# Kernel optimization log

Measured on AMD Instinct MI355X. Metric: run time of the kernel, lower is better.

The kernel has to match this reference:

```python
import jax, jax.numpy as jnp
import numpy as np

HIDDEN = 4096
NQ = 32        # query heads
NKV = 8        # kv heads
HD = 128       # head dim
EPS = 1e-6
BASE = 10000.0
T = 2048


def setup_inputs() -> dict:
    key = jax.random.key(0)
    ks = jax.random.split(key, 4)
    s = 0.02
    return {
        "hidden_states": jax.random.normal(ks[0], (T, HIDDEN), jnp.float32),
        "w_qkv": jax.random.normal(ks[1], ((NQ + 2 * NKV) * HD, HIDDEN), jnp.float32) * s,
        "q_norm_w": jnp.ones((HD,), jnp.float32),
        "k_norm_w": jnp.ones((HD,), jnp.float32),
        "w_o": jax.random.normal(ks[2], (HIDDEN, NQ * HD), jnp.float32) * s,
        "positions": jnp.arange(T, dtype=jnp.int64),
    }


def _rms_norm(x, w):
    # x: [T, H, D], normalize over last dim
    var = jnp.mean(jnp.square(x), axis=-1, keepdims=True)
    return x * jax.lax.rsqrt(var + EPS) * w


def _rope(x, positions):
    # neox-style: split halves. x: [T, H, D]
    half = HD // 2
    inv_freq = 1.0 / (BASE ** (jnp.arange(0, HD, 2, dtype=jnp.float32) / HD))  # [half]
    ang = positions.astype(jnp.float32)[:, None] * inv_freq  # [T, half]
    cos = jnp.cos(ang)[:, None, :]  # [T, 1, half]
    sin = jnp.sin(ang)[:, None, :]
    x1, x2 = x[..., :half], x[..., half:]
    return jnp.concatenate([x1 * cos - x2 * sin, x2 * cos + x1 * sin], axis=-1)


def reference(hidden_states, w_qkv, q_norm_w, k_norm_w, w_o, positions):
    t = hidden_states.shape[0]
    qkv = hidden_states @ w_qkv.T  # [T, (NQ+2*NKV)*HD]
    q, k, v = jnp.split(qkv, [NQ * HD, (NQ + NKV) * HD], axis=-1)
    q = _rms_norm(q.reshape(t, NQ, HD), q_norm_w)
    k = _rms_norm(k.reshape(t, NKV, HD), k_norm_w)
    v = v.reshape(t, NKV, HD)
    q = _rope(q, positions)
    k = _rope(k, positions)

    g = NQ // NKV
    qg = q.reshape(t, NKV, g, HD).transpose(1, 2, 0, 3)  # [NKV, g, T, HD]
    kt = k.transpose(1, 0, 2)  # [NKV, T, HD]
    vt = v.transpose(1, 0, 2)
    scale = HD ** -0.5
    scores = jnp.einsum('hgqd,hkd->hgqk', qg, kt) * scale  # [NKV, g, T, T]
    causal = positions[:, None] >= positions[None, :]  # [T, T]
    scores = jnp.where(causal[None, None], scores, jnp.float32(-1e30))
    p = jax.nn.softmax(scores, axis=-1)
    o = jnp.einsum('hgqk,hkd->hgqd', p, vt)  # [NKV, g, T, HD]
    o = o.transpose(2, 0, 1, 3).reshape(t, NQ * HD)
    return o @ w_o.T
```

## Files before the change

### kernel.cpp

```cpp
#include <hip/hip_runtime.h>
#include <hip/hip_bf16.h>

typedef float f32x4 __attribute__((ext_vector_type(4)));
typedef short s16x8 __attribute__((ext_vector_type(8)));
typedef short s16x4 __attribute__((ext_vector_type(4)));
typedef unsigned short u16;

#define HIDDEN 4096
#define NQ 32
#define NKV 8
#define HD 128
#define T_SEQ 2048
#define QKV_N ((NQ + 2 * NKV) * HD)

__device__ __forceinline__ u16 f2bf(float f) {
    union { float f; unsigned u; } v; v.f = f;
    unsigned r = v.u + 0x7FFFu + ((v.u >> 16) & 1u);
    return (u16)(r >> 16);
}
__device__ __forceinline__ float b2f(u16 h) {
    union { unsigned u; float f; } v; v.u = ((unsigned)h) << 16; return v.f;
}
__device__ __forceinline__ void gload_lds16(const u16* g, u16* l) {
    __builtin_amdgcn_global_load_lds(
        (const __attribute__((address_space(1))) unsigned int*)g,
        (__attribute__((address_space(3))) unsigned int*)l,
        16, 0, 0);
}
__device__ __forceinline__ int xcd_swz(int flat, int nwg) {
    return (flat & 7) * (nwg >> 3) + (flat >> 3);
}

__device__ __forceinline__ void conv8(const float* src, u16* dst, int i) {
    const float4 a = ((const float4*)src)[2 * i];
    const float4 b = ((const float4*)src)[2 * i + 1];
    s16x8 o;
    o[0] = (short)f2bf(a.x); o[1] = (short)f2bf(a.y);
    o[2] = (short)f2bf(a.z); o[3] = (short)f2bf(a.w);
    o[4] = (short)f2bf(b.x); o[5] = (short)f2bf(b.y);
    o[6] = (short)f2bf(b.z); o[7] = (short)f2bf(b.w);
    ((s16x8*)dst)[i] = o;
}
__global__ __launch_bounds__(256) void conv2_bf16_kern(
    const float* __restrict__ s1, u16* __restrict__ d1, int n1,
    const float* __restrict__ s2, u16* __restrict__ d2, int n2)
{
    for (int i = blockIdx.x * 256 + threadIdx.x; i < n1 + n2; i += gridDim.x * 256) {
        if (i < n1) conv8(s1, d1, i);
        else        conv8(s2, d2, i - n1);
    }
}

template<int OUT_BF16>
__global__ __launch_bounds__(256) void gemm_bt_bf16(
    const u16* __restrict__ A, const u16* __restrict__ B,
    void* __restrict__ Cv, int N, int K)
{
    __shared__ u16 As[2][128 * 32];
    __shared__ u16 Bs[2][128 * 32];
    const int tid = threadIdx.x, lane = tid & 63, wid = tid >> 6;
    const int wr = wid >> 1, wc = wid & 1, lg = lane >> 4, l15 = lane & 15;
    const int m0 = blockIdx.y * 128, n0 = blockIdx.x * 128;
    const int srow = wid * 32 + (lane >> 2);
    const int scol = (((lane & 3) ^ ((lane >> 3) & 3))) * 8;
    const u16* ga = &A[(size_t)(m0 + srow) * K + scol];
    const u16* gb = &B[(size_t)(n0 + srow) * K + scol];
    const int rsw = (lg ^ ((l15 >> 1) & 3)) * 8;

    f32x4 acc[4][4] = {};
    const int nk = K >> 5;

    auto stage = [&](int buf, int koff) {
        u16* la = &As[buf][wid * 1024];
        u16* lb = &Bs[buf][wid * 1024];
        gload_lds16(ga + koff, la);
        gload_lds16(ga + koff + 16 * K, la + 512);
        gload_lds16(gb + koff, lb);
        gload_lds16(gb + koff + 16 * K, lb + 512);
    };

    stage(0, 0);
    for (int kk = 0; kk < nk; ++kk) {
        const int cur = kk & 1;
        if (kk + 1 < nk) {
            stage(cur ^ 1, (kk + 1) * 32);
            asm volatile("s_waitcnt vmcnt(4)" ::: "memory");
        } else {
            asm volatile("s_waitcnt vmcnt(0)" ::: "memory");
        }
        __builtin_amdgcn_s_barrier();
        s16x8 af[4], bfr[4];
#pragma unroll
        for (int i = 0; i < 4; ++i) af[i]  = *(const s16x8*)&As[cur][(wr * 64 + i * 16 + l15) * 32 + rsw];
#pragma unroll
        for (int j = 0; j < 4; ++j) bfr[j] = *(const s16x8*)&Bs[cur][(wc * 64 + j * 16 + l15) * 32 + rsw];
#pragma unroll
        for (int i = 0; i < 4; ++i)
#pragma unroll
            for (int j = 0; j < 4; ++j)
                acc[i][j] = __builtin_amdgcn_mfma_f32_16x16x32_bf16(af[i], bfr[j], acc[i][j], 0, 0, 0);
        __builtin_amdgcn_s_barrier();
    }
#pragma unroll
    for (int i = 0; i < 4; ++i) {
        int r0 = m0 + wr * 64 + i * 16 + lg * 4;
#pragma unroll
        for (int j = 0; j < 4; ++j) {
            int cc = n0 + wc * 64 + j * 16 + l15;
#pragma unroll
            for (int r = 0; r < 4; ++r) {
                if (OUT_BF16)
                    ((u16*)Cv)[(size_t)(r0 + r) * N + cc] = f2bf(acc[i][j][r]);
                else
                    ((float*)Cv)[(size_t)(r0 + r) * N + cc] = acc[i][j][r];
            }
        }
    }
}

__global__ __launch_bounds__(256) void nr_vt_kern(
    const u16* __restrict__ qkv, const float* __restrict__ qw,
    const float* __restrict__ kw, u16* __restrict__ qr, u16* __restrict__ kr,
    u16* __restrict__ vt)
{
    __shared__ u16 Ts[128][66];
    const int id = blockIdx.x, tid = threadIdx.x;
    if (id < 20480) {
        const int t = id & 2047, h = (id >> 11) * 4 + (tid >> 6);
        const int i = tid & 63;
        const size_t rowbase = (size_t)t * QKV_N;
        const u16* src; const float* w; u16* dst;
        if (h < 32) {
            src = qkv + rowbase + h * HD; w = qw;
            dst = qr + ((size_t)h * T_SEQ + t) * HD;
        } else {
            int kh = h - 32;
            src = qkv + rowbase + NQ * HD + kh * HD; w = kw;
            dst = kr + ((size_t)kh * T_SEQ + t) * HD;
        }
        float x1 = b2f(src[i]), x2 = b2f(src[i + 64]);
        float ss = x1 * x1 + x2 * x2;
#pragma unroll
        for (int d = 32; d >= 1; d >>= 1) ss += __shfl_xor(ss, d);
        float rs = rsqrtf(ss * (1.0f / 128.0f) + 1e-6f);
        x1 *= rs * w[i];
        x2 *= rs * w[i + 64];
        float ang = (float)t * exp2f((float)i * -0.20762050593567985f);
        float sn, cs;
        sincosf(ang, &sn, &cs);
        dst[i]      = f2bf(x1 * cs - x2 * sn);
        dst[i + 64] = f2bf(x2 * cs + x1 * sn);
        return;
    }
    const int id2 = id - 20480;
    const int t0 = (id2 & 31) * 64, kh = id2 >> 5;
#pragma unroll
    for (int it = 0; it < 4; ++it) {
        int slot = tid + it * 256;
        int tl = slot >> 4, dc = (slot & 15) * 8;
        s16x8 v = *(const s16x8*)&qkv[(size_t)(t0 + tl) * QKV_N + (NQ + NKV) * HD + kh * HD + dc];
#pragma unroll
        for (int e = 0; e < 8; ++e) Ts[dc + e][tl] = (u16)v[e];
    }
    __syncthreads();
#pragma unroll
    for (int it = 0; it < 4; ++it) {
        int slot = tid + it * 256;
        int d = slot >> 3, c = (slot & 7) * 8;
        s16x8 v = *(const s16x8*)&Ts[d][c];
        *(s16x8*)&vt[((size_t)kh * HD + d) * T_SEQ + t0 + c] = v;
    }
}

#define KS(b, r, c) Ks[(b)][((r) << 7) + ((c) ^ (((r) & 7) << 3))]
#define VS(b, r, c) Vs[(b)][((r) << 6) + ((c) ^ (((r) & 7) << 3))]
#define PS(wv, r, c) Ps[((wv) << 10) + ((r) << 6) + ((c) ^ (((r) & 7) << 3))]

__global__ __launch_bounds__(512) void attn_kern(
    const u16* __restrict__ qr, const u16* __restrict__ kr,
    const u16* __restrict__ vt, u16* __restrict__ o,
    const float* __restrict__ wo, u16* __restrict__ wo_bf)
{
    __shared__ u16 Ks[2][64 * 128];
    __shared__ u16 Vs[2][128 * 64];
    __shared__ u16 Ps[8 * 16 * 64];
    const int tid = threadIdx.x, lane = tid & 63, w = tid >> 6;
    const int lg = lane >> 4, l15 = lane & 15;
    const int fb = (int)blockIdx.y * 8 + (int)blockIdx.x;
    const int flat = xcd_swz(fb, 256);
    const int qh = flat >> 3, bx = flat & 7;
    const int kvh = qh >> 2;
    const float scale2 = 0.08838834764831845f * 1.4426950408889634f;

    const int cvbase = fb * 8192 + tid;
    int cv = 0;
    float4 cva = {}, cvb = {};

    const int krow = tid >> 4, kcol = (tid & 15) * 8;
    const int vrow = tid >> 3, vcol = (tid & 7) * 8;
    const u16* krbase = kr + (size_t)kvh * T_SEQ * HD;
    const u16* vtbase = vt + (size_t)kvh * HD * T_SEQ;

    s16x8 kst[2], vst[2];
#define LOADKV(k0_) do { \
    kst[0] = *(const s16x8*)&krbase[(size_t)((k0_) + krow) * HD + kcol]; \
    kst[1] = *(const s16x8*)&krbase[(size_t)((k0_) + krow + 32) * HD + kcol]; \
    vst[0] = *(const s16x8*)&vtbase[(size_t)(vrow) * T_SEQ + (k0_) + vcol]; \
    vst[1] = *(const s16x8*)&vtbase[(size_t)(vrow + 64) * T_SEQ + (k0_) + vcol]; \
    } while (0)
#define WRITEKV(b) do { \
    *(s16x8*)&KS((b), krow, kcol) = kst[0]; \
    *(s16x8*)&KS((b), krow + 32, kcol) = kst[1]; \
    *(s16x8*)&VS((b), vrow, vcol) = vst[0]; \
    *(s16x8*)&VS((b), vrow + 64, vcol) = vst[1]; \
    } while (0)

    for (int half = 0; half < 2; ++half) {
        const int q0 = (half == 0) ? bx * 128 : (T_SEQ - 128) - bx * 128;
        s16x8 qf[4];
        {
            const u16* qb = qr + ((size_t)qh * T_SEQ + q0 + w * 16 + l15) * HD;
#pragma unroll
            for (int dc = 0; dc < 4; ++dc) qf[dc] = *(const s16x8*)&qb[dc * 32 + lg * 8];
        }
        f32x4 oacc[8] = {};
        float mQ = -1e30f, lsQ = 0.f;

        const int ktiles = (q0 >> 6) + 2;
        LOADKV(0);
        WRITEKV(0);
        __syncthreads();
        for (int kt = 0; kt < ktiles; ++kt) {
            const int k0 = kt * 64;
            const int cur = kt & 1;
            if (kt + 1 < ktiles) LOADKV(k0 + 64);

            if (cv <= 16) {
                if (cv > 0) {
                    s16x8 o8;
                    o8[0] = (short)f2bf(cva.x); o8[1] = (short)f2bf(cva.y);
                    o8[2] = (short)f2bf(cva.z); o8[3] = (short)f2bf(cva.w);
                    o8[4] = (short)f2bf(cvb.x); o8[5] = (short)f2bf(cvb.y);
                    o8[6] = (short)f2bf(cvb.z); o8[7] = (short)f2bf(cvb.w);
                    ((s16x8*)wo_bf)[cvbase + (cv - 1) * 512] = o8;
                }
                if (cv < 16) {
                    cva = ((const float4*)wo)[2 * (cvbase + cv * 512)];
                    cvb = ((const float4*)wo)[2 * (cvbase + cv * 512) + 1];
                }
                ++cv;
            }

            f32x4 sc[4] = {};
            __builtin_amdgcn_s_setprio(1);
#pragma unroll
            for (int nc = 0; nc < 4; ++nc)
#pragma unroll
                for (int dc = 0; dc < 4; ++dc) {
                    s16x8 kf = *(const s16x8*)&KS(cur, nc * 16 + l15, dc * 32 + lg * 8);
                    sc[nc] = __builtin_amdgcn_mfma_f32_16x16x32_bf16(kf, qf[dc], sc[nc], 0, 0, 0);
                }
            __builtin_amdgcn_s_setprio(0);

            const int qg = q0 + w * 16 + l15;
            const bool needMask = (k0 + 63) > (q0 + w * 16);
            float tm = -1e30f;
#pragma unroll
            for (int nc = 0; nc < 4; ++nc)
#pragma unroll
                for (int r = 0; r < 4; ++r) {
                    float v = sc[nc][r] * scale2;
                    int kg = k0 + nc * 16 + lg * 4 + r;
                    if (needMask && kg > qg) v = -1e30f;
                    sc[nc][r] = v;
                    tm = fmaxf(tm, v);
                }
            tm = fmaxf(tm, __shfl_xor(tm, 16));
            tm = fmaxf(tm, __shfl_xor(tm, 32));

            if (__any(tm > mQ + 8.0f)) {
                float mn = fmaxf(mQ, tm);
                float alpha = exp2f(mQ - mn);
                mQ = mn;
                lsQ *= alpha;
                float aq[4];
#pragma unroll
                for (int r = 0; r < 4; ++r) aq[r] = __shfl(alpha, lg * 4 + r);
#pragma unroll
                for (int dc = 0; dc < 8; ++dc)
#pragma unroll
                    for (int r = 0; r < 4; ++r) oacc[dc][r] *= aq[r];
            }

            float ts = 0.f;
#pragma unroll
            for (int nc = 0; nc < 4; ++nc) {
                s16x4 pk;
#pragma unroll
                for (int r = 0; r < 4; ++r) {
                    float e = exp2f(sc[nc][r] - mQ);
                    ts += e;
                    pk[r] = (short)f2bf(e);
                }
                *(s16x4*)&PS(w, l15, nc * 16 + lg * 4) = pk;
            }
            ts += __shfl_xor(ts, 16);
            ts += __shfl_xor(ts, 32);
            lsQ += ts;

            __builtin_amdgcn_s_setprio(1);
#pragma unroll
            for (int kc = 0; kc < 2; ++kc) {
                s16x8 pf = *(const s16x8*)&PS(w, l15, kc * 32 + lg * 8);
#pragma unroll
                for (int dc = 0; dc < 8; ++dc) {
                    s16x8 vf = *(const s16x8*)&VS(cur, dc * 16 + l15, kc * 32 + lg * 8);
                    oacc[dc] = __builtin_amdgcn_mfma_f32_16x16x32_bf16(pf, vf, oacc[dc], 0, 0, 0);
                }
            }
            __builtin_amdgcn_s_setprio(0);

            if (kt + 1 < ktiles) WRITEKV(cur ^ 1);
            __syncthreads();
        }
        float lq[4];
#pragma unroll
        for (int r = 0; r < 4; ++r) lq[r] = __shfl(lsQ, lg * 4 + r);
#pragma unroll
        for (int r = 0; r < 4; ++r) {
            float inv = 1.0f / lq[r];
            int trow = q0 + w * 16 + lg * 4 + r;
            u16* dst = o + (size_t)trow * (NQ * HD) + qh * HD;
#pragma unroll
            for (int dc = 0; dc < 8; ++dc) dst[dc * 16 + l15] = f2bf(oacc[dc][r] * inv);
        }
    }
#undef LOADKV
#undef WRITEKV
}

extern "C" void kernel_launch(void* const* d_in, const int* in_sizes, int n_in,
                              void* d_out, int out_size, void* d_ws, size_t ws_size,
                              hipStream_t stream)
{
    const float* hs   = (const float*)d_in[0];
    const float* wqkv = (const float*)d_in[1];
    const float* qw   = (const float*)d_in[2];
    const float* kw   = (const float*)d_in[3];
    const float* wo   = (const float*)d_in[4];
    float* out = (float*)d_out;

    char* ws = (char*)d_ws;
    u16* hs_bf   = (u16*)(ws);
    u16* ob      = (u16*)(ws);
    u16* wqkv_bf = (u16*)(ws + 16777216);
    u16* qr      = (u16*)(ws + 16777216);
    u16* kr      = (u16*)(ws + 33554432);
    u16* vt      = (u16*)(ws + 37748736);
    u16* wo_bf   = (u16*)(ws + 41943040);
    u16* qkv_bf  = (u16*)(ws + 67108864);

    conv2_bf16_kern<<<2048, 256, 0, stream>>>(
        hs, hs_bf, T_SEQ * HIDDEN / 8, wqkv, wqkv_bf, QKV_N * HIDDEN / 8);
    gemm_bt_bf16<1><<<dim3(QKV_N / 128, T_SEQ / 128), 256, 0, stream>>>(
        hs_bf, wqkv_bf, (void*)qkv_bf, QKV_N, HIDDEN);
    nr_vt_kern<<<20736, 256, 0, stream>>>(qkv_bf, qw, kw, qr, kr, vt);
    attn_kern<<<dim3(8, NQ), 512, 0, stream>>>(qr, kr, vt, ob, wo, wo_bf);
    gemm_bt_bf16<0><<<dim3(HIDDEN / 128, T_SEQ / 128), 256, 0, stream>>>(
        ob, wo_bf, (void*)out, HIDDEN, HIDDEN);
}
```

Baseline: 331.5 us.

## Fuse QK RMSNorm, RoPE and V transpose into QKV GEMM epilogue

```diff
diff --git a/kernel.cpp b/kernel.cpp
--- a/kernel.cpp
+++ b/kernel.cpp
@@ -51,15 +51,17 @@
     }
 }
 
-template<int OUT_BF16>
-__global__ __launch_bounds__(256) void gemm_bt_bf16(
+template<int MODE>
+__global__ __launch_bounds__(256) void gemm_bt(
     const u16* __restrict__ A, const u16* __restrict__ B,
-    void* __restrict__ Cv, int N, int K)
+    float* __restrict__ C, int N, int K,
+    const float* __restrict__ qw, const float* __restrict__ kw,
+    u16* __restrict__ qr, u16* __restrict__ kr, u16* __restrict__ vt)
 {
     __shared__ u16 As[2][128 * 32];
     __shared__ u16 Bs[2][128 * 32];
     const int tid = threadIdx.x, lane = tid & 63, wid = tid >> 6;
-    const int wr = wid >> 1, wc = wid & 1, lg = lane >> 4, l15 = lane & 15;
+    const int lg = lane >> 4, l15 = lane & 15;
     const int m0 = blockIdx.y * 128, n0 = blockIdx.x * 128;
     const int srow = wid * 32 + (lane >> 2);
     const int scol = (((lane & 3) ^ ((lane >> 3) & 3))) * 8;
@@ -67,7 +69,7 @@
     const u16* gb = &B[(size_t)(n0 + srow) * K + scol];
     const int rsw = (lg ^ ((l15 >> 1) & 3)) * 8;
 
-    f32x4 acc[4][4] = {};
+    f32x4 acc[2][8] = {};
     const int nk = K >> 5;
 
     auto stage = [&](int buf, int koff) {
@@ -89,86 +91,83 @@
             asm volatile("s_waitcnt vmcnt(0)" ::: "memory");
         }
         __builtin_amdgcn_s_barrier();
-        s16x8 af[4], bfr[4];
-#pragma unroll
-        for (int i = 0; i < 4; ++i) af[i]  = *(const s16x8*)&As[cur][(wr * 64 + i * 16 + l15) * 32 + rsw];
-#pragma unroll
-        for (int j = 0; j < 4; ++j) bfr[j] = *(const s16x8*)&Bs[cur][(wc * 64 + j * 16 + l15) * 32 + rsw];
-#pragma unroll
-        for (int i = 0; i < 4; ++i)
-#pragma unroll
-            for (int j = 0; j < 4; ++j)
+        s16x8 af[2], bfr[8];
+#pragma unroll
+        for (int i = 0; i < 2; ++i) af[i]  = *(const s16x8*)&As[cur][(wid * 32 + i * 16 + l15) * 32 + rsw];
+#pragma unroll
+        for (int j = 0; j < 8; ++j) bfr[j] = *(const s16x8*)&Bs[cur][(j * 16 + l15) * 32 + rsw];
+#pragma unroll
+        for (int i = 0; i < 2; ++i)
+#pragma unroll
+            for (int j = 0; j < 8; ++j)
                 acc[i][j] = __builtin_amdgcn_mfma_f32_16x16x32_bf16(af[i], bfr[j], acc[i][j], 0, 0, 0);
         __builtin_amdgcn_s_barrier();
     }
-#pragma unroll
-    for (int i = 0; i < 4; ++i) {
-        int r0 = m0 + wr * 64 + i * 16 + lg * 4;
-#pragma unroll
-        for (int j = 0; j < 4; ++j) {
-            int cc = n0 + wc * 64 + j * 16 + l15;
-#pragma unroll
-            for (int r = 0; r < 4; ++r) {
-                if (OUT_BF16)
-                    ((u16*)Cv)[(size_t)(r0 + r) * N + cc] = f2bf(acc[i][j][r]);
-                else
-                    ((float*)Cv)[(size_t)(r0 + r) * N + cc] = acc[i][j][r];
-            }
-        }
-    }
-}
-
-__global__ __launch_bounds__(256) void nr_vt_kern(
-    const u16* __restrict__ qkv, const float* __restrict__ qw,
-    const float* __restrict__ kw, u16* __restrict__ qr, u16* __restrict__ kr,
-    u16* __restrict__ vt)
-{
-    __shared__ u16 Ts[128][66];
-    const int id = blockIdx.x, tid = threadIdx.x;
-    if (id < 20480) {
-        const int t = id & 2047, h = (id >> 11) * 4 + (tid >> 6);
-        const int i = tid & 63;
-        const size_t rowbase = (size_t)t * QKV_N;
-        const u16* src; const float* w; u16* dst;
-        if (h < 32) {
-            src = qkv + rowbase + h * HD; w = qw;
-            dst = qr + ((size_t)h * T_SEQ + t) * HD;
-        } else {
-            int kh = h - 32;
-            src = qkv + rowbase + NQ * HD + kh * HD; w = kw;
-            dst = kr + ((size_t)kh * T_SEQ + t) * HD;
-        }
-        float x1 = b2f(src[i]), x2 = b2f(src[i + 64]);
-        float ss = x1 * x1 + x2 * x2;
-#pragma unroll
-        for (int d = 32; d >= 1; d >>= 1) ss += __shfl_xor(ss, d);
-        float rs = rsqrtf(ss * (1.0f / 128.0f) + 1e-6f);
-        x1 *= rs * w[i];
-        x2 *= rs * w[i + 64];
-        float ang = (float)t * exp2f((float)i * -0.20762050593567985f);
-        float sn, cs;
-        sincosf(ang, &sn, &cs);
-        dst[i]      = f2bf(x1 * cs - x2 * sn);
-        dst[i + 64] = f2bf(x2 * cs + x1 * sn);
+
+    const int tb = m0 + 32 * wid + lg * 4;
+    if (MODE == 0) {
+#pragma unroll
+        for (int i = 0; i < 2; ++i)
+#pragma unroll
+            for (int j = 0; j < 8; ++j) {
+                int cc = n0 + j * 16 + l15;
+#pragma unroll
+                for (int r = 0; r < 4; ++r)
+                    C[(size_t)(tb + i * 16 + r) * N + cc] = acc[i][j][r];
+            }
         return;
     }
-    const int id2 = id - 20480;
-    const int t0 = (id2 & 31) * 64, kh = id2 >> 5;
-#pragma unroll
-    for (int it = 0; it < 4; ++it) {
-        int slot = tid + it * 256;
-        int tl = slot >> 4, dc = (slot & 15) * 8;
-        s16x8 v = *(const s16x8*)&qkv[(size_t)(t0 + tl) * QKV_N + (NQ + NKV) * HD + kh * HD + dc];
-#pragma unroll
-        for (int e = 0; e < 8; ++e) Ts[dc + e][tl] = (u16)v[e];
-    }
-    __syncthreads();
-#pragma unroll
-    for (int it = 0; it < 4; ++it) {
-        int slot = tid + it * 256;
-        int d = slot >> 3, c = (slot & 7) * 8;
-        s16x8 v = *(const s16x8*)&Ts[d][c];
-        *(s16x8*)&vt[((size_t)kh * HD + d) * T_SEQ + t0 + c] = v;
+    const int head = n0 >> 7;
+    if (head >= 40) {
+        const int kvh = head - 40;
+#pragma unroll
+        for (int i = 0; i < 2; ++i)
+#pragma unroll
+            for (int j = 0; j < 8; ++j) {
+                int d = j * 16 + l15;
+                s16x4 pk;
+#pragma unroll
+                for (int r = 0; r < 4; ++r) pk[r] = (short)f2bf(acc[i][j][r]);
+                *(s16x4*)&vt[(size_t)(kvh * HD + d) * T_SEQ + tb + i * 16] = pk;
+            }
+        return;
+    }
+    const float* wgt = (head < 32) ? qw : kw;
+    u16* dst0 = (head < 32) ? (qr + (size_t)head * T_SEQ * HD)
+                            : (kr + (size_t)(head - 32) * T_SEQ * HD);
+    float wv[8];
+#pragma unroll
+    for (int j = 0; j < 8; ++j) wv[j] = wgt[j * 16 + l15];
+    float iff[4];
+#pragma unroll
+    for (int j = 0; j < 4; ++j)
+        iff[j] = exp2f((float)(j * 16 + l15) * -0.20762050593567985f);
+#pragma unroll
+    for (int i = 0; i < 2; ++i) {
+        float rs[4];
+#pragma unroll
+        for (int r = 0; r < 4; ++r) {
+            float s = 0.f;
+#pragma unroll
+            for (int j = 0; j < 8; ++j) s += acc[i][j][r] * acc[i][j][r];
+#pragma unroll
+            for (int d = 1; d < 16; d <<= 1) s += __shfl_xor(s, d);
+            rs[r] = rsqrtf(s * (1.0f / 128.0f) + 1e-6f);
+        }
+#pragma unroll
+        for (int r = 0; r < 4; ++r) {
+            int t = tb + i * 16 + r;
+            u16* dst = dst0 + (size_t)t * HD;
+#pragma unroll
+            for (int j = 0; j < 4; ++j) {
+                float sn, cs;
+                sincosf((float)t * iff[j], &sn, &cs);
+                float x1 = acc[i][j][r] * rs[r] * wv[j];
+                float x2 = acc[i][j + 4][r] * rs[r] * wv[j + 4];
+                dst[j * 16 + l15]      = f2bf(x1 * cs - x2 * sn);
+                dst[j * 16 + l15 + 64] = f2bf(x2 * cs + x1 * sn);
+            }
+        }
     }
 }
 
@@ -353,19 +352,17 @@
     char* ws = (char*)d_ws;
     u16* hs_bf   = (u16*)(ws);
     u16* ob      = (u16*)(ws);
-    u16* wqkv_bf = (u16*)(ws + 16777216);
     u16* qr      = (u16*)(ws + 16777216);
     u16* kr      = (u16*)(ws + 33554432);
     u16* vt      = (u16*)(ws + 37748736);
     u16* wo_bf   = (u16*)(ws + 41943040);
-    u16* qkv_bf  = (u16*)(ws + 67108864);
+    u16* wqkv_bf = (u16*)(ws + 41943040);
 
     conv2_bf16_kern<<<2048, 256, 0, stream>>>(
         hs, hs_bf, T_SEQ * HIDDEN / 8, wqkv, wqkv_bf, QKV_N * HIDDEN / 8);
-    gemm_bt_bf16<1><<<dim3(QKV_N / 128, T_SEQ / 128), 256, 0, stream>>>(
-        hs_bf, wqkv_bf, (void*)qkv_bf, QKV_N, HIDDEN);
-    nr_vt_kern<<<20736, 256, 0, stream>>>(qkv_bf, qw, kw, qr, kr, vt);
+    gemm_bt<2><<<dim3(QKV_N / 128, T_SEQ / 128), 256, 0, stream>>>(
+        hs_bf, wqkv_bf, nullptr, QKV_N, HIDDEN, qw, kw, qr, kr, vt);
     attn_kern<<<dim3(8, NQ), 512, 0, stream>>>(qr, kr, vt, ob, wo, wo_bf);
-    gemm_bt_bf16<0><<<dim3(HIDDEN / 128, T_SEQ / 128), 256, 0, stream>>>(
-        ob, wo_bf, (void*)out, HIDDEN, HIDDEN);
-}
+    gemm_bt<0><<<dim3(HIDDEN / 128, T_SEQ / 128), 256, 0, stream>>>(
+        ob, wo_bf, out, HIDDEN, HIDDEN, nullptr, nullptr, nullptr, nullptr, nullptr);
+}
```

Result: slower. 370.9 us (+11.9%).

## Replace QKV projection GEMM with 256x256-tile 8-wave phased pipelined kernel

Applied to the files above, without the earlier changes.

```diff
diff --git a/kernel.cpp b/kernel.cpp
--- a/kernel.cpp
+++ b/kernel.cpp
@@ -48,6 +48,101 @@
     for (int i = blockIdx.x * 256 + threadIdx.x; i < n1 + n2; i += gridDim.x * 256) {
         if (i < n1) conv8(s1, d1, i);
         else        conv8(s2, d2, i - n1);
+    }
+}
+
+__global__ __launch_bounds__(512) void gemm1_8ph(
+    const u16* __restrict__ A, const u16* __restrict__ B,
+    u16* __restrict__ C, int N, int K)
+{
+    __shared__ u16 As[2][256 * 64];
+    __shared__ u16 Bs[2][256 * 64];
+    const int tid = threadIdx.x, lane = tid & 63, wid = tid >> 6;
+    const int wr = wid >> 2, wc = wid & 3;
+    const int lg = lane >> 4, l15 = lane & 15;
+    const int m0 = blockIdx.y * 256, n0 = blockIdx.x * 256;
+    const int nk = K >> 6;
+    const int r8 = lane >> 3;
+    const int csw = ((lane & 7) ^ r8) * 8;
+
+    f32x4 acc[8][4] = {};
+
+    auto stageA = [&](int sl, int mh, int kt) {
+#pragma unroll
+        for (int l = 0; l < 2; ++l) {
+            int rb = l * 128 + mh * 64 + wid * 8;
+            gload_lds16(&A[(size_t)(m0 + rb + r8) * K + kt * 64 + csw],
+                        &As[sl][rb * 64]);
+        }
+    };
+    auto stageB = [&](int sl, int nh, int kt) {
+#pragma unroll
+        for (int l = 0; l < 2; ++l) {
+            int rb = (2 * l + (wid >> 2)) * 64 + nh * 32 + (wid & 3) * 8;
+            gload_lds16(&B[(size_t)(n0 + rb + r8) * K + kt * 64 + csw],
+                        &Bs[sl][rb * 64]);
+        }
+    };
+
+#define PHASE(s_, mh_, nh_, STAGE, WAIT)                                       \
+    {                                                                           \
+        s16x8 af[4][2], bq[2][2];                                               \
+        _Pragma("unroll") for (int mi = 0; mi < 4; ++mi)                        \
+        _Pragma("unroll") for (int kk = 0; kk < 2; ++kk)                        \
+            af[mi][kk] = *(const s16x8*)&As[s_][                                \
+                ((wr * 128 + (mh_) * 64 + mi * 16 + l15) << 6) +                \
+                (((lg + kk * 4) ^ (l15 & 7)) << 3)];                            \
+        _Pragma("unroll") for (int ni = 0; ni < 2; ++ni)                        \
+        _Pragma("unroll") for (int kk = 0; kk < 2; ++kk)                        \
+            bq[ni][kk] = *(const s16x8*)&Bs[s_][                                \
+                ((wc * 64 + (nh_) * 32 + ni * 16 + l15) << 6) +                 \
+                (((lg + kk * 4) ^ (l15 & 7)) << 3)];                            \
+        STAGE;                                                                  \
+        asm volatile("" ::: "memory");                                         \
+        __builtin_amdgcn_s_barrier();                                           \
+        __builtin_amdgcn_s_setprio(1);                                          \
+        _Pragma("unroll") for (int mi = 0; mi < 4; ++mi)                        \
+        _Pragma("unroll") for (int ni = 0; ni < 2; ++ni)                        \
+        _Pragma("unroll") for (int kk = 0; kk < 2; ++kk)                        \
+            acc[(mh_) * 4 + mi][(nh_) * 2 + ni] =                               \
+                __builtin_amdgcn_mfma_f32_16x16x32_bf16(                        \
+                    af[mi][kk], bq[ni][kk],                                     \
+                    acc[(mh_) * 4 + mi][(nh_) * 2 + ni], 0, 0, 0);              \
+        __builtin_amdgcn_s_setprio(0);                                          \
+        WAIT;                                                                   \
+        asm volatile("" ::: "memory");                                         \
+        __builtin_amdgcn_s_barrier();                                           \
+    }
+
+    stageA(0, 0, 0); stageA(0, 1, 0); stageB(0, 0, 0); stageB(0, 1, 0);
+    stageA(1, 0, 1); stageB(1, 0, 1);
+    asm volatile("s_waitcnt vmcnt(4)" ::: "memory");
+    __builtin_amdgcn_s_barrier();
+
+    for (int t = 0; t < nk; ++t) {
+        const int s = t & 1;
+        PHASE(s, 0, 0, { if (t + 1 < nk) stageA(s ^ 1, 1, t + 1); }, {});
+        PHASE(s, 0, 1, { if (t + 1 < nk) stageB(s ^ 1, 1, t + 1); }, {});
+        PHASE(s, 1, 0, { if (t + 2 < nk) stageA(s, 0, t + 2); }, {});
+        PHASE(s, 1, 1, { if (t + 2 < nk) stageB(s, 0, t + 2); },
+              { if (t + 2 < nk) asm volatile("s_waitcnt vmcnt(4)" ::: "memory");
+                else            asm volatile("s_waitcnt vmcnt(0)" ::: "memory"); });
+    }
+#undef PHASE
+
+#pragma unroll
+    for (int mh = 0; mh < 2; ++mh)
+#pragma unroll
+    for (int mi = 0; mi < 4; ++mi)
+#pragma unroll
+    for (int nh = 0; nh < 2; ++nh)
+#pragma unroll
+    for (int ni = 0; ni < 2; ++ni) {
+        int row0 = m0 + wr * 128 + mh * 64 + mi * 16 + lg * 4;
+        int col  = n0 + wc * 64 + nh * 32 + ni * 16 + l15;
+#pragma unroll
+        for (int r = 0; r < 4; ++r)
+            C[(size_t)(row0 + r) * N + col] = f2bf(acc[mh * 4 + mi][nh * 2 + ni][r]);
     }
 }
 
@@ -353,17 +448,17 @@
     char* ws = (char*)d_ws;
     u16* hs_bf   = (u16*)(ws);
     u16* ob      = (u16*)(ws);
-    u16* wqkv_bf = (u16*)(ws + 16777216);
     u16* qr      = (u16*)(ws + 16777216);
     u16* kr      = (u16*)(ws + 33554432);
     u16* vt      = (u16*)(ws + 37748736);
     u16* wo_bf   = (u16*)(ws + 41943040);
+    u16* wqkv_bf = (u16*)(ws + 41943040);
     u16* qkv_bf  = (u16*)(ws + 67108864);
 
     conv2_bf16_kern<<<2048, 256, 0, stream>>>(
         hs, hs_bf, T_SEQ * HIDDEN / 8, wqkv, wqkv_bf, QKV_N * HIDDEN / 8);
-    gemm_bt_bf16<1><<<dim3(QKV_N / 128, T_SEQ / 128), 256, 0, stream>>>(
-        hs_bf, wqkv_bf, (void*)qkv_bf, QKV_N, HIDDEN);
+    gemm1_8ph<<<dim3(QKV_N / 256, T_SEQ / 256), 512, 0, stream>>>(
+        hs_bf, wqkv_bf, qkv_bf, QKV_N, HIDDEN);
     nr_vt_kern<<<20736, 256, 0, stream>>>(qkv_bf, qw, kw, qr, kr, vt);
     attn_kern<<<dim3(8, NQ), 512, 0, stream>>>(qr, kr, vt, ob, wo, wo_bf);
     gemm_bt_bf16<0><<<dim3(HIDDEN / 128, T_SEQ / 128), 256, 0, stream>>>(
```

Measured after the change: 344.2 us. 1.04x slower.
